# Kernel tuning notes

Measured on AMD Instinct MI355X. Metric: run time of the kernel, lower is better.

## Reference

```python
import jax, jax.numpy as jnp
import numpy as np

NEG_SLOPE = 0.2  # PyG GATConv leaky_relu slope
N_NODE = 1000   # nodes per graph (= n_nodes ctor arg = lstm1 input_size)
BATCH = 32      # num_graphs
C = 32          # in_channels == GAT out_channels per head
HEADS = 8
E = 384000      # total edges over the batched graph
H1, H2 = 32, 128
N_PRED = 2
N = N_NODE * BATCH


def _lstm(x_seq, W_ih, W_hh, b_ih, b_hh):
    # x_seq: [T, B, In]; PyTorch gate order i,f,g,o
    B = x_seq.shape[1]
    Hd = W_hh.shape[1]
    h0 = jnp.zeros((B, Hd), x_seq.dtype)

    def step(carry, x_t):
        h, c = carry
        g = x_t @ W_ih.T + h @ W_hh.T + b_ih + b_hh
        i, f, gg, o = jnp.split(g, 4, axis=-1)
        c = jax.nn.sigmoid(f) * c + jax.nn.sigmoid(i) * jnp.tanh(gg)
        h = jax.nn.sigmoid(o) * jnp.tanh(c)
        return (h, c), h

    (_, _), hs = jax.lax.scan(step, (h0, h0), x_seq)
    return hs


def setup_inputs() -> dict:
    key = jax.random.key(0)
    ks = jax.random.split(key, 20)
    inp = {}
    inp["x"] = jax.random.normal(ks[0], (N, C), jnp.float32)
    inp["src"] = jax.random.randint(ks[1], (E,), 0, N)
    inp["dst"] = jax.random.randint(ks[2], (E,), 0, N)
    inp["batch_size"] = BATCH
    # GATConv params (concat=False: mean over heads)
    inp["W_gat"] = jax.random.normal(ks[3], (C, HEADS * C), jnp.float32) * 0.1
    inp["a_src"] = jax.random.normal(ks[4], (HEADS, C), jnp.float32) * 0.1
    inp["a_dst"] = jax.random.normal(ks[5], (HEADS, C), jnp.float32) * 0.1
    inp["b_gat"] = jnp.zeros((C,), jnp.float32)
    # LSTM1: input N_NODE -> hidden 32
    inp["W_ih1"] = jax.random.normal(ks[6], (4 * H1, N_NODE), jnp.float32) * 0.05
    inp["W_hh1"] = jax.random.normal(ks[7], (4 * H1, H1), jnp.float32) * 0.1
    inp["b_ih1"] = jnp.zeros((4 * H1,), jnp.float32)
    inp["b_hh1"] = jnp.zeros((4 * H1,), jnp.float32)
    # LSTM2: input 32 -> hidden 128 (repaired from buggy source)
    inp["W_ih2"] = jax.random.normal(ks[8], (4 * H2, H1), jnp.float32) * 0.1
    inp["W_hh2"] = jax.random.normal(ks[9], (4 * H2, H2), jnp.float32) * 0.08
    inp["b_ih2"] = jnp.zeros((4 * H2,), jnp.float32)
    inp["b_hh2"] = jnp.zeros((4 * H2,), jnp.float32)
    # Linear head: 128 -> n_nodes * n_pred
    inp["W_lin"] = jax.random.normal(ks[10], (N_NODE * N_PRED, H2), jnp.float32) * 0.08
    inp["b_lin"] = jnp.zeros((N_NODE * N_PRED,), jnp.float32)
    return inp


def reference(x, src, dst, batch_size, W_gat, a_src, a_dst, b_gat,
              W_ih1, W_hh1, b_ih1, b_hh1, W_ih2, W_hh2, b_ih2, b_hh2,
              W_lin, b_lin):
    n, c = x.shape
    h = a_src.shape[0]
    # --- GATConv ---
    x_lin = (x @ W_gat).reshape(n, h, c)               # [N, H, C]
    asrc = jnp.einsum('nhc,hc->nh', x_lin, a_src)      # [N, H]
    adst = jnp.einsum('nhc,hc->nh', x_lin, a_dst)
    e = jax.nn.leaky_relu(asrc[src] + adst[dst], NEG_SLOPE)   # [E, H]
    m = jax.ops.segment_max(e, dst, num_segments=n)
    m = jnp.where(jnp.isfinite(m), m, 0.0)             # isolated nodes
    ew = jnp.exp(e - m[dst])
    denom = jax.ops.segment_sum(ew, dst, num_segments=n)
    alpha = ew / jnp.maximum(denom[dst], 1e-16)        # segment softmax
    agg = jax.ops.segment_sum(alpha[:, :, None] * x_lin[src], dst, num_segments=n)
    out = agg.mean(axis=1) + b_gat                     # concat=False -> head mean; [N, C]
    # --- reshape: seq over feature dim, LSTM input = nodes-per-graph ---
    n_node = n // batch_size
    seq = jnp.moveaxis(out.reshape(batch_size, n_node, c), 2, 0)  # [C, B, n_node]
    h1 = _lstm(seq, W_ih1, W_hh1, b_ih1, b_hh1)
    h2 = _lstm(h1, W_ih2, W_hh2, b_ih2, b_hh2)
    last = h2[-1]                                       # [B, 128]
    y = last @ W_lin.T + b_lin                          # [B, n_node*n_pred]
    return y.reshape(batch_size * n_node, -1)           # [B*n_node, n_pred]
```

## Files before the change

### kernel.cpp

```cpp
#include <hip/hip_runtime.h>
#include <hip/hip_fp16.h>
#include <math.h>

#define NEG_SLOPE 0.2f

__device__ __forceinline__ float sigm(float x) { return 1.0f / (1.0f + __expf(-x)); }
__device__ __forceinline__ float tanh_fast(float x) {
    float xc = fminf(fmaxf(x, -15.0f), 15.0f);
    float e2 = __expf(2.0f * xc);
    return (e2 - 1.0f) / (e2 + 1.0f);
}
__device__ __forceinline__ float lrelu(float x) { return (x > 0.0f) ? x : NEG_SLOPE * x; }

typedef _Float16 h2v __attribute__((ext_vector_type(2)));
__device__ __forceinline__ float fdot2h(h2v a, h2v b, float c) {
#if __has_builtin(__builtin_amdgcn_fdot2)
    return __builtin_amdgcn_fdot2(a, b, c, false);
#else
    return (float)a[0] * (float)b[0] + (float)a[1] * (float)b[1] + c;
#endif
}

__global__ void k_zero(int* __restrict__ deg, int N) {
    int i = blockIdx.x * 256 + threadIdx.x;
    if (i < N) deg[i] = 0;
}

__global__ void k_hist(const int* __restrict__ dst, int* __restrict__ deg, int E) {
    int e = blockIdx.x * 256 + threadIdx.x;
    if (e < E) atomicAdd(deg + dst[e], 1);
}

__global__ __launch_bounds__(256) void k_scan1(const int* __restrict__ deg,
                                               int* __restrict__ blksum, int N) {
    __shared__ int s[256];
    int tid = threadIdx.x;
    int i = blockIdx.x * 256 + tid;
    int v = (i < N) ? deg[i] : 0;
    s[tid] = v;
    __syncthreads();
    #pragma unroll
    for (int off = 128; off > 0; off >>= 1) {
        if (tid < off) s[tid] += s[tid + off];
        __syncthreads();
    }
    if (tid == 0) blksum[blockIdx.x] = s[0];
}

__global__ __launch_bounds__(256) void k_scan2(const int* __restrict__ blksum,
                                               int* __restrict__ blkoff, int nb) {
    __shared__ int s[256];
    int tid = threadIdx.x;
    int v = (tid < nb) ? blksum[tid] : 0;
    s[tid] = v;
    __syncthreads();
    for (int off = 1; off < 256; off <<= 1) {
        int t = (tid >= off) ? s[tid - off] : 0;
        __syncthreads();
        s[tid] += t;
        __syncthreads();
    }
    if (tid < nb) blkoff[tid] = s[tid] - v;
}

__global__ __launch_bounds__(256) void k_scan3(const int* __restrict__ deg,
                                               const int* __restrict__ blkoff,
                                               int* __restrict__ rowptr,
                                               int* __restrict__ cursor, int N, int E) {
    __shared__ int s[256];
    int tid = threadIdx.x;
    int i = blockIdx.x * 256 + tid;
    int v = (i < N) ? deg[i] : 0;
    s[tid] = v;
    __syncthreads();
    for (int off = 1; off < 256; off <<= 1) {
        int t = (tid >= off) ? s[tid - off] : 0;
        __syncthreads();
        s[tid] += t;
        __syncthreads();
    }
    int excl = s[tid] - v + blkoff[blockIdx.x];
    if (i < N) { rowptr[i] = excl; cursor[i] = excl; }
    if (i == N - 1) rowptr[N] = E;
}

__global__ void k_scatter(const int* __restrict__ src, const int* __restrict__ dst,
                          int* __restrict__ cursor, int* __restrict__ csr_src, int E) {
    int e = blockIdx.x * 256 + threadIdx.x;
    if (e < E) {
        int pos = atomicAdd(cursor + dst[e], 1);
        csr_src[pos] = src[e];
    }
}

__global__ void k_pre(const float* __restrict__ W_gat, const float* __restrict__ a_src,
                      const float* __restrict__ a_dst, float* __restrict__ wa) {
    int tid = threadIdx.x;
    int k = tid >> 3, h = tid & 7;
    float s1 = 0.0f, s2 = 0.0f;
    for (int c = 0; c < 32; ++c) {
        float wv = W_gat[k * 256 + h * 32 + c];
        s1 += wv * a_src[h * 32 + c];
        s2 += wv * a_dst[h * 32 + c];
    }
    wa[tid] = s1;
    wa[256 + tid] = s2;
}

__global__ __launch_bounds__(256) void k_att(const float* __restrict__ x,
                                             const float* __restrict__ wa,
                                             float* __restrict__ asrc,
                                             float* __restrict__ adst) {
    __shared__ float xs[32 * 33];
    __shared__ float was[256], wad[256];
    int tid = threadIdx.x;
    int n0 = blockIdx.x * 32;
    for (int i = tid; i < 1024; i += 256) {
        int nl = i >> 5, k = i & 31;
        xs[nl * 33 + k] = x[(size_t)(n0 + nl) * 32 + k];
    }
    was[tid] = wa[tid];
    wad[tid] = wa[256 + tid];
    __syncthreads();
    int nl = tid >> 3, h = tid & 7;
    float s1 = 0.0f, s2 = 0.0f;
    #pragma unroll
    for (int k = 0; k < 32; ++k) {
        float xv = xs[nl * 33 + k];
        s1 += xv * was[k * 8 + h];
        s2 += xv * wad[k * 8 + h];
    }
    asrc[(size_t)(n0 + nl) * 8 + h] = s1;
    adst[(size_t)(n0 + nl) * 8 + h] = s2;
}

__global__ __launch_bounds__(256) void k_gat(
    const int* __restrict__ rowptr, const int* __restrict__ csr_src,
    const float* __restrict__ asrc, const float* __restrict__ adst,
    const float* __restrict__ x, float* __restrict__ z, int N) {
    int w = (blockIdx.x * 256 + threadIdx.x) >> 6;
    int lane = threadIdx.x & 63;
    if (w >= N) return;
    int r0 = rowptr[w], r1 = rowptr[w + 1];
    int h = lane >> 3, kq = lane & 7;
    float ad = adst[w * 8 + h];
    float4 acc = make_float4(0.0f, 0.0f, 0.0f, 0.0f);
    float den = 0.0f;
    const float4* x4 = (const float4*)x;
    for (int i = r0; i < r1; ++i) {
        int s = csr_src[i];
        float ew = __expf(lrelu(asrc[s * 8 + h] + ad));
        float4 xv = x4[(size_t)s * 8 + kq];
        acc.x += ew * xv.x; acc.y += ew * xv.y;
        acc.z += ew * xv.z; acc.w += ew * xv.w;
        den += ew;
    }
    float inv = 1.0f / fmaxf(den, 1e-16f);
    float4 r = make_float4(acc.x * inv, acc.y * inv, acc.z * inv, acc.w * inv);
    ((float4*)z)[(size_t)w * 64 + lane] = r;
}

__global__ __launch_bounds__(256) void k_zw(
    const float* __restrict__ z, const float* __restrict__ W_gat,
    const float* __restrict__ b_gat, float* __restrict__ gatT, int N, int n_node) {
    int gw = (blockIdx.x * 256 + threadIdx.x) >> 6;
    int lane = threadIdx.x & 63;
    int chalf = gw & 1;
    int nset = gw >> 1;
    int c = chalf * 16 + (lane & 15);
    int sl = lane >> 4;
    float wcol[64];
    #pragma unroll
    for (int i = 0; i < 64; ++i) {
        int k = i & 31, hh = sl * 2 + (i >> 5);
        wcol[i] = 0.125f * W_gat[k * 256 + hh * 32 + c];
    }
    float bg = b_gat[c];
    const float4* z4 = (const float4*)z;
    for (int it = 0; it < 8; ++it) {
        int n = nset * 8 + it;
        if (n >= N) break;
        float p = 0.0f;
        #pragma unroll
        for (int k4 = 0; k4 < 16; ++k4) {
            float4 zv = z4[(size_t)n * 64 + sl * 16 + k4];
            p += zv.x * wcol[4 * k4] + zv.y * wcol[4 * k4 + 1]
               + zv.z * wcol[4 * k4 + 2] + zv.w * wcol[4 * k4 + 3];
        }
        p += __shfl_xor(p, 16, 64);
        p += __shfl_xor(p, 32, 64);
        if (lane < 16) {
            int b = n / n_node, kk = n - b * n_node;
            gatT[((size_t)b * 32 + c) * n_node + kk] = p + bg;
        }
    }
}

__global__ __launch_bounds__(256) void k_wt(const float* __restrict__ W,
                                            float* __restrict__ Wt, int n_node) {
    __shared__ float tle[32][33];
    int kt = blockIdx.x & 31;
    int gt = blockIdx.x >> 5;
    int tid = threadIdx.x;
    for (int i = tid; i < 1024; i += 256) {
        int gl = i >> 5, kl = i & 31;
        int g = gt * 32 + gl, k = kt * 32 + kl;
        tle[gl][kl] = (k < n_node) ? W[(size_t)g * n_node + k] : 0.0f;
    }
    __syncthreads();
    for (int i = tid; i < 1024; i += 256) {
        int kl = i >> 5, gl = i & 31;
        int k = kt * 32 + kl, g = gt * 32 + gl;
        if (k < n_node) Wt[(size_t)k * 128 + g] = tle[gl][kl];
    }
}

__global__ __launch_bounds__(256) void k_p1(
    const float* __restrict__ gatT, const float* __restrict__ Wt,
    const float* __restrict__ b_ih1, const float* __restrict__ b_hh1,
    float* __restrict__ P1, int n_node, int B) {
    __shared__ __align__(16) float Arow[2][1024];
    __shared__ __align__(16) float part[4][2][128];
    int blk = blockIdx.x;
    int b = blk >> 4;
    int tq = blk & 15;
    int tid = threadIdx.x;
    const float* A0 = gatT + ((size_t)b * 32 + tq * 2) * n_node;
    #pragma unroll
    for (int r = 0; r < 2; ++r)
        for (int i = tid; i < n_node; i += 256)
            Arow[r][i] = A0[(size_t)r * n_node + i];
    __syncthreads();

    int g4 = tid & 31;
    int tloc = (tid >> 5) & 1;
    int ks = tid >> 6;
    int kq = n_node >> 2;
    int k0 = ks * kq;
    const float4* Wt4 = (const float4*)Wt;
    float4 acc = make_float4(0.0f, 0.0f, 0.0f, 0.0f);
    #pragma unroll 4
    for (int k = 0; k < kq; ++k) {
        float4 w = Wt4[(size_t)(k0 + k) * 32 + g4];
        float a = Arow[tloc][k0 + k];
        acc.x += w.x * a; acc.y += w.y * a;
        acc.z += w.z * a; acc.w += w.w * a;
    }
    *(float4*)&part[ks][tloc][g4 * 4] = acc;
    __syncthreads();

    int tl = tid >> 7, g = tid & 127;
    float s = part[0][tl][g] + part[1][tl][g] + part[2][tl][g] + part[3][tl][g]
            + b_ih1[g] + b_hh1[g];
    int t = tq * 2 + tl;
    P1[((size_t)t * B + b) * 128 + g] = s;
}

__global__ __launch_bounds__(256) void k_lstm(
    const float* __restrict__ P1, const float* __restrict__ W_hh1,
    const float* __restrict__ W_ih2, const float* __restrict__ W_hh2,
    const float* __restrict__ b_ih2, const float* __restrict__ b_hh2,
    float* __restrict__ h2finT, int B, int T) {
    __shared__ __align__(16) float P1s[32][128];
    __shared__ __align__(16) float h1s[32];
    __shared__ __align__(16) float g1s[128];
    __shared__ __align__(16) float h1all[32][32];
    __shared__ __align__(16) float P2l[512 * 33];
    __shared__ __align__(16) __half hbuf[2][128];
    int tid = threadIdx.x, b = blockIdx.x;
    int lane = tid & 63, wv = tid >> 6;
    int n = wv * 32 + (lane & 31);
    int hl = lane >> 5;

    for (int i = tid; i < 4096; i += 256) {
        int t = i >> 7, g = i & 127;
        P1s[t][g] = P1[((size_t)t * B + b) * 128 + g];
    }
    float4 w1[8];
    if (tid < 128) {
        const float4* W = (const float4*)(W_hh1 + (size_t)tid * 32);
        #pragma unroll
        for (int j = 0; j < 8; ++j) w1[j] = W[j];
    }
    if (tid < 32) h1s[tid] = 0.0f;
    if (tid < 128) hbuf[0][tid] = __float2half(0.0f);
    float c1 = 0.0f;
    __syncthreads();

    for (int t = 0; t < 32; ++t) {
        if (tid < 128) {
            float acc = P1s[t][tid];
            const float4* hp = (const float4*)h1s;
            #pragma unroll
            for (int j = 0; j < 8; ++j) {
                float4 h = hp[j], w = w1[j];
                acc += w.x * h.x + w.y * h.y + w.z * h.z + w.w * h.w;
            }
            g1s[tid] = acc;
        }
        __syncthreads();
        if (tid < 32) {
            float i_ = sigm(g1s[tid]), f_ = sigm(g1s[32 + tid]);
            float g_ = tanh_fast(g1s[64 + tid]), o_ = sigm(g1s[96 + tid]);
            c1 = f_ * c1 + i_ * g_;
            float h = o_ * tanh_fast(c1);
            h1s[tid] = h;
            h1all[t][tid] = h;
        }
        __syncthreads();
    }

    {
        float4 wi[4][8];
        float bias[4];
        #pragma unroll
        for (int g = 0; g < 4; ++g) {
            int r = g * 128 + n;
            const float4* Wi = (const float4*)(W_ih2 + (size_t)r * 32);
            #pragma unroll
            for (int j = 0; j < 8; ++j) wi[g][j] = Wi[j];
            bias[g] = b_ih2[r] + b_hh2[r];
        }
        for (int t = 0; t < 32; ++t) {
            const float4* hp = (const float4*)h1all[t];
            float4 hv[8];
            #pragma unroll
            for (int j = 0; j < 8; ++j) hv[j] = hp[j];
            #pragma unroll
            for (int g = 0; g < 4; ++g) {
                float p = bias[g];
                #pragma unroll
                for (int j = 0; j < 8; ++j) {
                    float4 w = wi[g][j], h = hv[j];
                    p += w.x * h.x + w.y * h.y + w.z * h.z + w.w * h.w;
                }
                if (hl == 0) P2l[(g * 128 + n) * 33 + t] = p;
            }
        }
    }
    __syncthreads();

    h2v wh[4][32];
    #pragma unroll
    for (int g = 0; g < 4; ++g) {
        const float4* Wr = (const float4*)(W_hh2 + (size_t)(g * 128 + n) * 128 + hl * 64);
        #pragma unroll
        for (int j = 0; j < 16; ++j) {
            float4 w = Wr[j];
            h2v t0, t1;
            t0[0] = (_Float16)w.x; t0[1] = (_Float16)w.y;
            t1[0] = (_Float16)w.z; t1[1] = (_Float16)w.w;
            wh[g][2 * j] = t0;
            wh[g][2 * j + 1] = t1;
        }
    }
    float c2 = 0.0f;

    for (int t = 0; t < T; ++t) {
        const uint4* hc4 = (const uint4*)hbuf[t & 1];
        uint4 hvv[8];
        #pragma unroll
        for (int j = 0; j < 8; ++j) hvv[j] = hc4[hl * 8 + j];
        float s[4];
        #pragma unroll
        for (int g = 0; g < 4; ++g) {
            float a0 = 0.0f, a1 = 0.0f, a2 = 0.0f, a3 = 0.0f;
            #pragma unroll
            for (int j = 0; j < 8; ++j) {
                const h2v* hp = reinterpret_cast<const h2v*>(&hvv[j]);
                a0 = fdot2h(wh[g][4 * j],     hp[0], a0);
                a1 = fdot2h(wh[g][4 * j + 1], hp[1], a1);
                a2 = fdot2h(wh[g][4 * j + 2], hp[2], a2);
                a3 = fdot2h(wh[g][4 * j + 3], hp[3], a3);
            }
            s[g] = (a0 + a1) + (a2 + a3);
        }
        #pragma unroll
        for (int g = 0; g < 4; ++g) {
            s[g] += __shfl_xor(s[g], 32, 64);
            s[g] += P2l[(g * 128 + n) * 33 + t];
        }
        float i_ = sigm(s[0]), f_ = sigm(s[1]);
        float g_ = tanh_fast(s[2]), o_ = sigm(s[3]);
        c2 = f_ * c2 + i_ * g_;
        float h = o_ * tanh_fast(c2);
        if (hl == 0) {
            hbuf[(t + 1) & 1][n] = __float2half(h);
            if (t == T - 1) h2finT[n * 32 + b] = h;
        }
        __syncthreads();
    }
}

__global__ __launch_bounds__(256) void k_fin(
    const float* __restrict__ h2finT, const float* __restrict__ W_lin,
    const float* __restrict__ b_lin, float* __restrict__ out, int n_node, int B) {
    __shared__ __align__(16) float hs[128];
    int b = blockIdx.x >> 3;
    int kc = blockIdx.x & 7;
    int tid = threadIdx.x;
    if (tid < 128) hs[tid] = h2finT[tid * 32 + b];
    __syncthreads();
    int outdim = n_node * 2;
    int kk = kc * 256 + tid;
    if (kk < outdim) {
        float acc = b_lin[kk];
        const float4* W4 = (const float4*)(W_lin + (size_t)kk * 128);
        const float4* h4 = (const float4*)hs;
        #pragma unroll 8
        for (int j = 0; j < 32; ++j) {
            float4 w = W4[j], h = h4[j];
            acc += w.x * h.x + w.y * h.y + w.z * h.z + w.w * h.w;
        }
        out[(size_t)b * outdim + kk] = acc;
    }
}

extern "C" void kernel_launch(void* const* d_in, const int* in_sizes, int n_in,
                              void* d_out, int out_size, void* d_ws, size_t ws_size,
                              hipStream_t stream) {
    const float* x     = (const float*)d_in[0];
    const int*   src   = (const int*)d_in[1];
    const int*   dst   = (const int*)d_in[2];
    const float* W_gat = (const float*)d_in[4];
    const float* a_src = (const float*)d_in[5];
    const float* a_dst = (const float*)d_in[6];
    const float* b_gat = (const float*)d_in[7];
    const float* W_ih1 = (const float*)d_in[8];
    const float* W_hh1 = (const float*)d_in[9];
    const float* b_ih1 = (const float*)d_in[10];
    const float* b_hh1 = (const float*)d_in[11];
    const float* W_ih2 = (const float*)d_in[12];
    const float* W_hh2 = (const float*)d_in[13];
    const float* b_ih2 = (const float*)d_in[14];
    const float* b_hh2 = (const float*)d_in[15];
    const float* W_lin = (const float*)d_in[16];
    const float* b_lin = (const float*)d_in[17];

    int N = in_sizes[0] / 32;
    int E = in_sizes[1];
    int n_node = in_sizes[8] / 128;
    int B = N / n_node;
    int T = 32;

    float* ws = (float*)d_ws;
    float* z      = ws;
    float* asrc   = z + (size_t)N * 256;
    float* adst   = asrc + (size_t)N * 8;
    float* gatT   = adst + (size_t)N * 8;
    float* P1     = gatT + (size_t)N * 32;
    float* h1g    = P1 + (size_t)T * B * 128;
    float* P2g    = h1g + (size_t)B * 1024;
    float* h2finT = P2g + (size_t)B * 16384;
    float* wa     = h2finT + 128 * 32;
    int* deg     = (int*)(wa + 512);
    int* cursor  = deg + N;
    int* rowptr  = cursor + N;
    int* csr_src = rowptr + N + 1;
    int* blksum  = csr_src + E;
    int* blkoff  = blksum + 256;
    float* Wt    = (float*)(((uintptr_t)(blkoff + 256) + 255) & ~(uintptr_t)255);

    int nb = (N + 255) / 256;

    k_wt<<<128, 256, 0, stream>>>(W_ih1, Wt, n_node);
    k_zero<<<(N + 255) / 256, 256, 0, stream>>>(deg, N);
    k_hist<<<(E + 255) / 256, 256, 0, stream>>>(dst, deg, E);
    k_scan1<<<nb, 256, 0, stream>>>(deg, blksum, N);
    k_scan2<<<1, 256, 0, stream>>>(blksum, blkoff, nb);
    k_scan3<<<nb, 256, 0, stream>>>(deg, blkoff, rowptr, cursor, N, E);
    k_scatter<<<(E + 255) / 256, 256, 0, stream>>>(src, dst, cursor, csr_src, E);
    k_pre<<<1, 256, 0, stream>>>(W_gat, a_src, a_dst, wa);
    k_att<<<N / 32, 256, 0, stream>>>(x, wa, asrc, adst);
    k_gat<<<(N * 64 + 255) / 256, 256, 0, stream>>>(rowptr, csr_src, asrc, adst,
                                                    x, z, N);
    k_zw<<<2000, 256, 0, stream>>>(z, W_gat, b_gat, gatT, N, n_node);
    k_p1<<<B * 16, 256, 0, stream>>>(gatT, Wt, b_ih1, b_hh1, P1, n_node, B);
    k_lstm<<<B, 256, 0, stream>>>(P1, W_hh1, W_ih2, W_hh2, b_ih2, b_hh2,
                                  h2finT, B, T);
    k_fin<<<B * 8, 256, 0, stream>>>(h2finT, W_lin, b_lin, (float*)d_out, n_node, B);
}
```

Before: 238.4 us.

## Pipeline LSTM1 and LSTM2 time steps in one wider block

The fused LSTM kernel now runs with 640 threads. 128 threads compute LSTM1 gates for step s while 512 threads compute LSTM2 for step s-1, each thread owning one gate row of W_hh2 and W_ih2 in registers. The separate serial phases for LSTM1, the input projection and LSTM2 are merged into one wavefront-pipelined loop, which removes the P2 shared buffer and the cross-half shuffle. The cost is more threads per block, heavier register use per thread (64 half2 plus 8 float4 weights), and a gate exchange through lane shuffles.

```diff
diff --git a/kernel.cpp b/kernel.cpp
--- a/kernel.cpp
+++ b/kernel.cpp
@@ -256,7 +256,7 @@
     P1[((size_t)t * B + b) * 128 + g] = s;
 }
 
-__global__ __launch_bounds__(256) void k_lstm(
+__global__ __launch_bounds__(640) void k_lstm(
     const float* __restrict__ P1, const float* __restrict__ W_hh1,
     const float* __restrict__ W_ih2, const float* __restrict__ W_hh2,
     const float* __restrict__ b_ih2, const float* __restrict__ b_hh2,
@@ -265,128 +265,102 @@
     __shared__ __align__(16) float h1s[32];
     __shared__ __align__(16) float g1s[128];
     __shared__ __align__(16) float h1all[32][32];
-    __shared__ __align__(16) float P2l[512 * 33];
     __shared__ __align__(16) __half hbuf[2][128];
     int tid = threadIdx.x, b = blockIdx.x;
-    int lane = tid & 63, wv = tid >> 6;
-    int n = wv * 32 + (lane & 31);
-    int hl = lane >> 5;
-
-    for (int i = tid; i < 4096; i += 256) {
+
+    for (int i = tid; i < 4096; i += 640) {
         int t = i >> 7, g = i & 127;
         P1s[t][g] = P1[((size_t)t * B + b) * 128 + g];
     }
+
     float4 w1[8];
     if (tid < 128) {
         const float4* W = (const float4*)(W_hh1 + (size_t)tid * 32);
         #pragma unroll
         for (int j = 0; j < 8; ++j) w1[j] = W[j];
     }
+
+    int tid2 = tid - 128;
+    int gt = tid2 & 3, n = tid2 >> 2;
+    int g_idx = gt * 128 + n;
+    h2v wh[64];
+    float4 wi[8];
+    float bias = 0.0f;
+    if (tid >= 128) {
+        const float4* Wr = (const float4*)(W_hh2 + (size_t)g_idx * 128);
+        #pragma unroll
+        for (int j = 0; j < 32; ++j) {
+            float4 w = Wr[j];
+            h2v t0, t1;
+            t0[0] = (_Float16)w.x; t0[1] = (_Float16)w.y;
+            t1[0] = (_Float16)w.z; t1[1] = (_Float16)w.w;
+            wh[2 * j] = t0;
+            wh[2 * j + 1] = t1;
+        }
+        const float4* Wi = (const float4*)(W_ih2 + (size_t)g_idx * 32);
+        #pragma unroll
+        for (int j = 0; j < 8; ++j) wi[j] = Wi[j];
+        bias = b_ih2[g_idx] + b_hh2[g_idx];
+    }
+
     if (tid < 32) h1s[tid] = 0.0f;
-    if (tid < 128) hbuf[0][tid] = __float2half(0.0f);
-    float c1 = 0.0f;
-    __syncthreads();
-
-    for (int t = 0; t < 32; ++t) {
+    if (tid >= 128 && tid < 256) hbuf[0][tid - 128] = __float2half(0.0f);
+    float c1 = 0.0f, c2 = 0.0f;
+    __syncthreads();
+
+    for (int s = 0; s <= T; ++s) {
         if (tid < 128) {
-            float acc = P1s[t][tid];
-            const float4* hp = (const float4*)h1s;
+            if (s < T) {
+                float acc = P1s[s][tid];
+                const float4* hp = (const float4*)h1s;
+                #pragma unroll
+                for (int j = 0; j < 8; ++j) {
+                    float4 h = hp[j], w = w1[j];
+                    acc += w.x * h.x + w.y * h.y + w.z * h.z + w.w * h.w;
+                }
+                g1s[tid] = acc;
+            }
+        } else if (s >= 1) {
+            int t2 = s - 1;
+            const float4* hp1 = (const float4*)h1all[t2];
+            float p = bias;
             #pragma unroll
             for (int j = 0; j < 8; ++j) {
-                float4 h = hp[j], w = w1[j];
-                acc += w.x * h.x + w.y * h.y + w.z * h.z + w.w * h.w;
+                float4 w = wi[j], h = hp1[j];
+                p += w.x * h.x + w.y * h.y + w.z * h.z + w.w * h.w;
             }
-            g1s[tid] = acc;
-        }
-        __syncthreads();
-        if (tid < 32) {
+            const uint4* hc4 = (const uint4*)hbuf[t2 & 1];
+            float a0 = 0.0f, a1 = 0.0f, a2 = 0.0f, a3 = 0.0f;
+            #pragma unroll
+            for (int j = 0; j < 16; ++j) {
+                uint4 hv = hc4[j];
+                const h2v* hp = reinterpret_cast<const h2v*>(&hv);
+                a0 = fdot2h(wh[4 * j],     hp[0], a0);
+                a1 = fdot2h(wh[4 * j + 1], hp[1], a1);
+                a2 = fdot2h(wh[4 * j + 2], hp[2], a2);
+                a3 = fdot2h(wh[4 * j + 3], hp[3], a3);
+            }
+            float acc = p + ((a0 + a1) + (a2 + a3));
+            float v1 = __shfl_xor(acc, 1, 64);
+            float v2 = __shfl_xor(acc, 2, 64);
+            float v3 = __shfl_xor(acc, 3, 64);
+            if (gt == 0) {
+                float i_ = sigm(acc), f_ = sigm(v1);
+                float g_ = tanh_fast(v2), o_ = sigm(v3);
+                c2 = f_ * c2 + i_ * g_;
+                float h = o_ * tanh_fast(c2);
+                hbuf[(t2 + 1) & 1][n] = __float2half(h);
+                if (t2 == T - 1) h2finT[n * 32 + b] = h;
+            }
+        }
+        __syncthreads();
+        if (tid < 32 && s < T) {
             float i_ = sigm(g1s[tid]), f_ = sigm(g1s[32 + tid]);
             float g_ = tanh_fast(g1s[64 + tid]), o_ = sigm(g1s[96 + tid]);
             c1 = f_ * c1 + i_ * g_;
             float h = o_ * tanh_fast(c1);
             h1s[tid] = h;
-            h1all[t][tid] = h;
-        }
-        __syncthreads();
-    }
-
-    {
-        float4 wi[4][8];
-        float bias[4];
-        #pragma unroll
-        for (int g = 0; g < 4; ++g) {
-            int r = g * 128 + n;
-            const float4* Wi = (const float4*)(W_ih2 + (size_t)r * 32);
-            #pragma unroll
-            for (int j = 0; j < 8; ++j) wi[g][j] = Wi[j];
-            bias[g] = b_ih2[r] + b_hh2[r];
-        }
-        for (int t = 0; t < 32; ++t) {
-            const float4* hp = (const float4*)h1all[t];
-            float4 hv[8];
-            #pragma unroll
-            for (int j = 0; j < 8; ++j) hv[j] = hp[j];
-            #pragma unroll
-            for (int g = 0; g < 4; ++g) {
-                float p = bias[g];
-                #pragma unroll
-                for (int j = 0; j < 8; ++j) {
-                    float4 w = wi[g][j], h = hv[j];
-                    p += w.x * h.x + w.y * h.y + w.z * h.z + w.w * h.w;
-                }
-                if (hl == 0) P2l[(g * 128 + n) * 33 + t] = p;
-            }
-        }
-    }
-    __syncthreads();
-
-    h2v wh[4][32];
-    #pragma unroll
-    for (int g = 0; g < 4; ++g) {
-        const float4* Wr = (const float4*)(W_hh2 + (size_t)(g * 128 + n) * 128 + hl * 64);
-        #pragma unroll
-        for (int j = 0; j < 16; ++j) {
-            float4 w = Wr[j];
-            h2v t0, t1;
-            t0[0] = (_Float16)w.x; t0[1] = (_Float16)w.y;
-            t1[0] = (_Float16)w.z; t1[1] = (_Float16)w.w;
-            wh[g][2 * j] = t0;
-            wh[g][2 * j + 1] = t1;
-        }
-    }
-    float c2 = 0.0f;
-
-    for (int t = 0; t < T; ++t) {
-        const uint4* hc4 = (const uint4*)hbuf[t & 1];
-        uint4 hvv[8];
-        #pragma unroll
-        for (int j = 0; j < 8; ++j) hvv[j] = hc4[hl * 8 + j];
-        float s[4];
-        #pragma unroll
-        for (int g = 0; g < 4; ++g) {
-            float a0 = 0.0f, a1 = 0.0f, a2 = 0.0f, a3 = 0.0f;
-            #pragma unroll
-            for (int j = 0; j < 8; ++j) {
-                const h2v* hp = reinterpret_cast<const h2v*>(&hvv[j]);
-                a0 = fdot2h(wh[g][4 * j],     hp[0], a0);
-                a1 = fdot2h(wh[g][4 * j + 1], hp[1], a1);
-                a2 = fdot2h(wh[g][4 * j + 2], hp[2], a2);
-                a3 = fdot2h(wh[g][4 * j + 3], hp[3], a3);
-            }
-            s[g] = (a0 + a1) + (a2 + a3);
-        }
-        #pragma unroll
-        for (int g = 0; g < 4; ++g) {
-            s[g] += __shfl_xor(s[g], 32, 64);
-            s[g] += P2l[(g * 128 + n) * 33 + t];
-        }
-        float i_ = sigm(s[0]), f_ = sigm(s[1]);
-        float g_ = tanh_fast(s[2]), o_ = sigm(s[3]);
-        c2 = f_ * c2 + i_ * g_;
-        float h = o_ * tanh_fast(c2);
-        if (hl == 0) {
-            hbuf[(t + 1) & 1][n] = __float2half(h);
-            if (t == T - 1) h2finT[n * 32 + b] = h;
+            h1all[s][tid] = h;
         }
         __syncthreads();
     }
@@ -476,7 +450,7 @@
                                                     x, z, N);
     k_zw<<<2000, 256, 0, stream>>>(z, W_gat, b_gat, gatT, N, n_node);
     k_p1<<<B * 16, 256, 0, stream>>>(gatT, Wt, b_ih1, b_hh1, P1, n_node, B);
-    k_lstm<<<B, 256, 0, stream>>>(P1, W_hh1, W_ih2, W_hh2, b_ih2, b_hh2,
+    k_lstm<<<B, 640, 0, stream>>>(P1, W_hh1, W_ih2, W_hh2, b_ih2, b_hh2,
                                   h2finT, B, T);
     k_fin<<<B * 8, 256, 0, stream>>>(h2finT, W_lin, b_lin, (float*)d_out, n_node, B);
 }
```

Measured after the change: 239.8 us. About the same (+0.6%).
